# Kernel optimization log

Measured on AMD Instinct MI355X. Metric: run time of the kernel, lower is better.

## Reference

```python
import math
import jax, jax.numpy as jnp
import numpy as np

NUM_HEADS = 16
EMBED = 1024
B, T = 2, 2048


def setup_inputs() -> dict:
    key = jax.random.key(0)
    k1, k2 = jax.random.split(key)
    x = jax.random.normal(k1, (B, T, EMBED), dtype=jnp.float32)
    # kaiming-uniform-style init for [num_heads*embed, embed]
    bound = 1.0 / math.sqrt(NUM_HEADS * EMBED)
    weight = jax.random.uniform(k2, (NUM_HEADS * EMBED, EMBED), dtype=jnp.float32,
                                minval=-bound, maxval=bound)
    return {"x": x, "weight": weight}


def reference(x, weight):
    b, t, c = x.shape
    nh = NUM_HEADS
    hs = c // nh
    # b t (nh hs) -> b nh t hs
    y = x.reshape(b, t, nh, hs).transpose(0, 2, 1, 3)
    # scores: [b, nh, t, t], scaled by sqrt(hs) (yt.shape[-2] == hs)
    scores = jnp.einsum('bhtk,bhsk->bhts', y, y) / math.sqrt(hs)
    attn = jax.nn.softmax(scores, axis=-1)
    # value is raw x broadcast per head; contract without materializing the repeat
    o = jnp.einsum('bhts,bsc->bhtc', attn, x)          # [b, nh, t, c]
    o = o.transpose(0, 2, 1, 3).reshape(b, t, nh * c)  # b nh t c -> b t (nh c)
    return o @ weight                                   # [b, t, c]
```

## Files before the change

### kernel.cpp

```cpp
#include <hip/hip_runtime.h>
#include <hip/hip_bf16.h>


typedef __hip_bfloat16 bf16;
typedef __bf16 bf16x8 __attribute__((ext_vector_type(8)));
typedef float f32x4 __attribute__((ext_vector_type(4)));

#define B_ 2
#define T_ 2048
#define C_ 1024
#define H_ 16
#define D_ 16384
#define E_ 1024
#define KZ_ 8

__device__ __forceinline__ void load_lds16(const void* g, void* l) {
  __builtin_amdgcn_global_load_lds(
      (const __attribute__((address_space(1))) void*)g,
      (__attribute__((address_space(3))) void*)l, 16, 0, 0);
}

__device__ __forceinline__ unsigned pack2(float a, float b) {
  union { bf16 h[2]; unsigned u; } p;
  p.h[0] = __float2bfloat16(a);
  p.h[1] = __float2bfloat16(b);
  return p.u;
}

__global__ __launch_bounds__(256) void transpose_cast_kernel(
    const float* __restrict__ in, bf16* __restrict__ out, int rows, int cols) {
  __shared__ float tile[32][33];
  size_t zoff = (size_t)blockIdx.z * rows * cols;
  int c0 = blockIdx.x * 32, r0 = blockIdx.y * 32;
  int tx = threadIdx.x, ty = threadIdx.y;
  for (int i = ty; i < 32; i += 8)
    tile[i][tx] = in[zoff + (size_t)(r0 + i) * cols + c0 + tx];
  __syncthreads();
  for (int i = ty; i < 32; i += 8)
    out[zoff + (size_t)(c0 + i) * rows + r0 + tx] = __float2bfloat16(tile[tx][i]);
}

__global__ __launch_bounds__(256) void xh_cast_kernel(
    const float* __restrict__ x, bf16* __restrict__ xh) {
  int bt = blockIdx.x;
  int b = bt >> 11, t = bt & (T_ - 1);
  float4 v = ((const float4*)(x + (size_t)bt * C_))[threadIdx.x];
  int c = threadIdx.x * 4;
  int h = c >> 6, k = c & 63;
  bf16* o = xh + ((size_t)(b * H_ + h) * T_ + t) * 64 + k;
  o[0] = __float2bfloat16(v.x);
  o[1] = __float2bfloat16(v.y);
  o[2] = __float2bfloat16(v.z);
  o[3] = __float2bfloat16(v.w);
}

__global__ __launch_bounds__(256) void reduce_kernel(
    const bf16* __restrict__ p, float* __restrict__ out, int n8) {
  int i = blockIdx.x * 256 + threadIdx.x;
  if (i >= n8) return;
  float a[8] = {};
#pragma unroll
  for (int z = 0; z < KZ_; ++z) {
    bf16x8 v = ((const bf16x8*)(p + (size_t)z * n8 * 8))[i];
#pragma unroll
    for (int k = 0; k < 8; ++k) a[k] += (float)v[k];
  }
  float4 lo = make_float4(a[0], a[1], a[2], a[3]);
  float4 hi = make_float4(a[4], a[5], a[6], a[7]);
  ((float4*)out)[2 * i] = lo;
  ((float4*)out)[2 * i + 1] = hi;
}

__global__ __launch_bounds__(256) void scores_kernel(
    const bf16* __restrict__ xh,
    bf16* __restrict__ P,
    float* __restrict__ lsum) {
  int L = blockIdx.x;
  int z = blockIdx.y;
  int ti = 0, rem = L;
  while (rem >= H_ - ti) { rem -= H_ - ti; ++ti; }
  int tj = ti + rem;

  const bf16* A = xh + (size_t)z * T_ * 64;
  bf16* Pz = P + (size_t)z * T_ * T_;
  size_t row0 = (size_t)ti * 128, col0 = (size_t)tj * 128;

  __shared__ bf16 lds_a[128 * 64];
  __shared__ bf16 lds_b[128 * 64];
  int t = threadIdx.x;

  const bf16* ga = A + (row0 + (t >> 3)) * 64 + (t & 7) * 8;
  const bf16* gb = A + (col0 + (t >> 3)) * 64 + (t & 7) * 8;
#pragma unroll
  for (int q = 0; q < 4; ++q) {
    load_lds16(ga + q * 32 * 64, lds_a + t * 8 + q * 2048);
    load_lds16(gb + q * 32 * 64, lds_b + t * 8 + q * 2048);
  }
  __syncthreads();

  int lane = t & 63, w = t >> 6;
  int wm = (w & 1) * 64, wn = (w >> 1) * 64;
  int lr = lane & 15, lq = lane >> 4;
  const int a_off = (wm + lr) * 64 + lq * 8;
  const int b_off = (wn + lr) * 64 + lq * 8;

  f32x4 acc[4][4] = {};
#pragma unroll
  for (int kh = 0; kh < 2; ++kh) {
    bf16x8 af[4], bfr[4];
#pragma unroll
    for (int i = 0; i < 4; ++i)
      af[i] = *(const bf16x8*)&lds_a[a_off + kh * 32 + i * 16 * 64];
#pragma unroll
    for (int j = 0; j < 4; ++j)
      bfr[j] = *(const bf16x8*)&lds_b[b_off + kh * 32 + j * 16 * 64];
#pragma unroll
    for (int i = 0; i < 4; ++i)
#pragma unroll
      for (int j = 0; j < 4; ++j)
        acc[i][j] = __builtin_amdgcn_mfma_f32_16x16x32_bf16(af[i], bfr[j],
                                                            acc[i][j], 0, 0, 0);
  }

  float rs[4][4];
  float cs[4];
#pragma unroll
  for (int i2 = 0; i2 < 4; ++i2)
#pragma unroll
    for (int reg = 0; reg < 4; ++reg) rs[i2][reg] = 0.f;
#pragma unroll
  for (int j2 = 0; j2 < 4; ++j2) cs[j2] = 0.f;

#pragma unroll
  for (int i2 = 0; i2 < 4; ++i2) {
    size_t rb = row0 + wm + i2 * 16 + lq * 4;
#pragma unroll
    for (int j2 = 0; j2 < 4; ++j2) {
      size_t c = col0 + wn + j2 * 16 + lr;
      float e[4];
#pragma unroll
      for (int reg = 0; reg < 4; ++reg) {
        e[reg] = __expf(acc[i2][j2][reg] * 0.125f);
        rs[i2][reg] += e[reg];
        cs[j2] += e[reg];
        float nb = __shfl_xor(e[reg], 1);
        if ((lr & 1) == 0)
          *(unsigned*)&Pz[(rb + reg) * T_ + c] = pack2(e[reg], nb);
      }
      uint2 mv;
      mv.x = pack2(e[0], e[1]);
      mv.y = pack2(e[2], e[3]);
      *(uint2*)&Pz[c * T_ + rb] = mv;
    }
  }

#pragma unroll
  for (int i2 = 0; i2 < 4; ++i2)
#pragma unroll
    for (int reg = 0; reg < 4; ++reg) {
#pragma unroll
      for (int off = 1; off < 16; off <<= 1)
        rs[i2][reg] += __shfl_xor(rs[i2][reg], off);
    }
  if (lr == 0) {
#pragma unroll
    for (int i2 = 0; i2 < 4; ++i2) {
      size_t rb = row0 + wm + i2 * 16 + lq * 4;
#pragma unroll
      for (int reg = 0; reg < 4; ++reg)
        atomicAdd(&lsum[(size_t)z * T_ + rb + reg], rs[i2][reg]);
    }
  }
  if (ti != tj) {
#pragma unroll
    for (int j2 = 0; j2 < 4; ++j2) {
      cs[j2] += __shfl_xor(cs[j2], 16);
      cs[j2] += __shfl_xor(cs[j2], 32);
    }
    if (lq == 0) {
#pragma unroll
      for (int j2 = 0; j2 < 4; ++j2) {
        size_t c = col0 + wn + j2 * 16 + lr;
        atomicAdd(&lsum[(size_t)z * T_ + c], cs[j2]);
      }
    }
  }
}

template <int MODE, int SWZ>
__global__ __launch_bounds__(256, 4) void gemm_bt_kernel(
    const bf16* __restrict__ A, long long a_zstride, int lda,
    const bf16* __restrict__ BT, long long b_zstride, int ldb,
    void* __restrict__ Cout, int ldc, long long c_zflat,
    const float* __restrict__ lsum, int lzs, int K) {
  __shared__ bf16 lds_a[128 * 32];
  __shared__ bf16 lds_b[128 * 32];
  int t = threadIdx.x;

  int bx = blockIdx.x, by = blockIdx.y, bz = blockIdx.z;
  if (SWZ) {
    int gx = gridDim.x, gy = gridDim.y, gz = gridDim.z;
    int S = gy * gz, nb = gx * S;
    if (((S & 7) == 0) && ((nb & 7) == 0)) {
      int L = bx + gx * (by + gy * bz);
      int xcd = L & 7, m = L >> 3, spx = S >> 3;
      int col = m % gx, sl = m / gx;
      int strip = xcd * spx + sl;
      bx = col; by = strip % gy; bz = strip / gy;
    }
  }

  const bf16* Ab = A + (size_t)bz * a_zstride;
  const bf16* Bb = BT + (size_t)bz * b_zstride;
  size_t row0 = (size_t)by * 128;
  size_t col0 = (size_t)bx * 128;

  const bf16* ga = Ab + (row0 + (t >> 2)) * (size_t)lda + (t & 3) * 8;
  const bf16* gb = Bb + (col0 + (t >> 2)) * (size_t)ldb + (t & 3) * 8;
  bf16* la = lds_a + t * 8;
  bf16* lb = lds_b + t * 8;

  f32x4 acc[4][4] = {};
  int lane = t & 63;
  int w = t >> 6;
  int wm = (w & 1) * 64, wn = (w >> 1) * 64;
  int lr = lane & 15, lq = lane >> 4;
  const int a_off0 = (wm + lr) * 32 + lq * 8;
  const int b_off0 = (wn + lr) * 32 + lq * 8;

  for (int k0 = 0; k0 < K; k0 += 32) {
    load_lds16(ga, la);
    load_lds16(ga + 64 * (size_t)lda, la + 64 * 32);
    load_lds16(gb, lb);
    load_lds16(gb + 64 * (size_t)ldb, lb + 64 * 32);
    ga += 32;
    gb += 32;
    __syncthreads();

    bf16x8 af[4], bfr[4];
#pragma unroll
    for (int i = 0; i < 4; ++i)
      af[i] = *(const bf16x8*)&lds_a[a_off0 + i * 16 * 32];
#pragma unroll
    for (int j = 0; j < 4; ++j)
      bfr[j] = *(const bf16x8*)&lds_b[b_off0 + j * 16 * 32];
#pragma unroll
    for (int i = 0; i < 4; ++i)
#pragma unroll
      for (int j = 0; j < 4; ++j)
        acc[i][j] = __builtin_amdgcn_mfma_f32_16x16x32_bf16(af[i], bfr[j],
                                                            acc[i][j], 0, 0, 0);
    __syncthreads();
  }

  size_t cbase = (size_t)bz * c_zflat + col0;
#pragma unroll
  for (int i = 0; i < 4; ++i) {
    size_t r = row0 + wm + i * 16 + lq * 4;
    float4 inv4 = make_float4(1.f, 1.f, 1.f, 1.f);
    if (MODE == 3) {
      float4 lv = *(const float4*)&lsum[(size_t)bz * lzs + r];
      inv4 = make_float4(1.f / lv.x, 1.f / lv.y, 1.f / lv.z, 1.f / lv.w);
    }
#pragma unroll
    for (int j = 0; j < 4; ++j) {
      size_t c = cbase + wn + j * 16 + lr;
#pragma unroll
      for (int reg = 0; reg < 4; ++reg) {
        float v = acc[i][j][reg];
        if (MODE == 3) {
          float iv = reg == 0 ? inv4.x : reg == 1 ? inv4.y : reg == 2 ? inv4.z
                                                                      : inv4.w;
          v *= iv;
        }
        float nb = __shfl_xor(v, 1);
        if ((lr & 1) == 0) {
          size_t idx = (r + reg) * (size_t)ldc + c;
          *(unsigned*)&((bf16*)Cout)[idx] = pack2(v, nb);
        }
      }
    }
  }
}

extern "C" void kernel_launch(void* const* d_in, const int* in_sizes, int n_in,
                              void* d_out, int out_size, void* d_ws,
                              size_t ws_size, hipStream_t stream) {
  const float* x = (const float*)d_in[0];
  const float* wgt = (const float*)d_in[1];
  float* out = (float*)d_out;

  bf16* xbT = (bf16*)d_ws;
  bf16* wbT = xbT + (size_t)B_ * C_ * T_;
  bf16* xh = wbT + (size_t)E_ * D_;
  bf16* Obuf = xh + (size_t)B_ * H_ * T_ * 64;
  float* lsum = (float*)(Obuf + (size_t)B_ * T_ * D_);
  bf16* P = (bf16*)(lsum + (size_t)16 * T_);
  bf16* partials = P;

  transpose_cast_kernel<<<dim3(C_ / 32, T_ / 32, B_), dim3(32, 8), 0, stream>>>(
      x, xbT, T_, C_);
  transpose_cast_kernel<<<dim3(E_ / 32, D_ / 32, 1), dim3(32, 8), 0, stream>>>(
      wgt, wbT, D_, E_);
  xh_cast_kernel<<<B_ * T_, 256, 0, stream>>>(x, xh);

  size_t fixed_bytes = ((size_t)B_ * C_ * T_ + (size_t)E_ * D_ +
                        (size_t)B_ * H_ * T_ * 64 + (size_t)B_ * T_ * D_) * 2 +
                       (size_t)16 * T_ * 4;
  int Hs = 16;
  while (Hs > 1 && fixed_bytes + (size_t)Hs * T_ * T_ * 2 > ws_size) Hs >>= 1;

  for (int b = 0; b < B_; ++b) {
    for (int h0 = 0; h0 < H_; h0 += Hs) {
      const bf16* xhb = xh + (size_t)(b * H_ + h0) * T_ * 64;
      hipMemsetAsync(lsum, 0, (size_t)Hs * T_ * sizeof(float), stream);
      scores_kernel<<<dim3(136, Hs), 256, 0, stream>>>(xhb, P, lsum);
      gemm_bt_kernel<3, 1><<<dim3(C_ / 128, T_ / 128, Hs), 256, 0, stream>>>(
          P, (long long)T_ * T_, T_, xbT + (size_t)b * C_ * T_, 0LL, T_,
          (void*)(Obuf + (size_t)b * T_ * D_ + (size_t)h0 * C_), D_,
          (long long)C_, lsum, T_, T_);
    }
  }
  gemm_bt_kernel<1, 1><<<dim3(E_ / 128, (B_ * T_) / 128, KZ_), 256, 0,
                         stream>>>(Obuf, (long long)(D_ / KZ_), D_, wbT,
                                   (long long)(D_ / KZ_), D_, (void*)partials,
                                   E_, (long long)B_ * T_ * E_, nullptr, 0,
                                   D_ / KZ_);
  reduce_kernel<<<(B_ * T_ * E_ / 8 + 255) / 256, 256, 0, stream>>>(
      partials, out, B_ * T_ * E_ / 8);
}
```

Baseline: 759.0 us.

## Replace 128x128 GEMM with double-buffered 256x256 tile kernel using swizzled LDS

Result: no change. 744.2 us (-1.9%).

```diff
diff --git a/kernel.cpp b/kernel.cpp
--- a/kernel.cpp
+++ b/kernel.cpp
@@ -187,15 +187,76 @@
   }
 }
 
+template <int IH, int JH>
+__device__ __forceinline__ void quad(f32x4 (&acc)[8][4], const bf16x8 (&aR)[8],
+                                     const bf16x8 (&bR)[4]) {
+#pragma unroll
+  for (int i = 0; i < 4; ++i)
+#pragma unroll
+    for (int jj = 0; jj < 2; ++jj)
+#pragma unroll
+      for (int kk = 0; kk < 2; ++kk)
+        acc[IH * 4 + i][JH * 2 + jj] = __builtin_amdgcn_mfma_f32_16x16x32_bf16(
+            aR[i * 2 + kk], bR[jj * 2 + kk], acc[IH * 4 + i][JH * 2 + jj], 0, 0,
+            0);
+}
+
+#define STAGE_A(bufi, h, tau)                                                 \
+  do {                                                                        \
+    load_lds16(Ab + offA[(h)*2 + 0] + (tau)*64,                               \
+               &ldsA[bufi][(((h)*512) + t) * 8]);                             \
+    load_lds16(Ab + offA[(h)*2 + 1] + (tau)*64,                               \
+               &ldsA[bufi][((1024 + (h)*512) + t) * 8]);                      \
+  } while (0)
+
+#define STAGE_B(bufi, h, tau)                                                 \
+  do {                                                                        \
+    load_lds16(Bb + offB[(h)*2 + 0] + (tau)*64,                               \
+               &ldsB[bufi][(((t >> 8) * 512) + (h)*256 + (t & 255)) * 8]);    \
+    load_lds16(                                                               \
+        Bb + offB[(h)*2 + 1] + (tau)*64,                                      \
+        &ldsB[bufi][((((t + 512) >> 8) * 512) + (h)*256 + (t & 255)) * 8]);   \
+  } while (0)
+
+#define RD_A(dst, d, add)                                                     \
+  do {                                                                        \
+    dst[0] = *(const bf16x8*)&ldsA[d][aoff[0] + (add)];                       \
+    dst[1] = *(const bf16x8*)&ldsA[d][aoff[1] + (add)];                       \
+    dst[2] = *(const bf16x8*)&ldsA[d][aoff[2] + (add)];                       \
+    dst[3] = *(const bf16x8*)&ldsA[d][aoff[3] + (add)];                       \
+    dst[4] = *(const bf16x8*)&ldsA[d][aoff[4] + (add)];                       \
+    dst[5] = *(const bf16x8*)&ldsA[d][aoff[5] + (add)];                       \
+    dst[6] = *(const bf16x8*)&ldsA[d][aoff[6] + (add)];                       \
+    dst[7] = *(const bf16x8*)&ldsA[d][aoff[7] + (add)];                       \
+  } while (0)
+
+#define RD_B(dst, d, add)                                                     \
+  do {                                                                        \
+    dst[0] = *(const bf16x8*)&ldsB[d][boff[0] + (add)];                       \
+    dst[1] = *(const bf16x8*)&ldsB[d][boff[1] + (add)];                       \
+    dst[2] = *(const bf16x8*)&ldsB[d][boff[2] + (add)];                       \
+    dst[3] = *(const bf16x8*)&ldsB[d][boff[3] + (add)];                       \
+  } while (0)
+
+#define PHASE_SYNC()                                                          \
+  __builtin_amdgcn_sched_barrier(0);                                          \
+  __builtin_amdgcn_s_barrier();                                               \
+  asm volatile("s_waitcnt lgkmcnt(0)" ::: "memory");                          \
+  __builtin_amdgcn_sched_barrier(0)
+
+#define PHASE_END()                                                           \
+  __builtin_amdgcn_sched_barrier(0);                                          \
+  __builtin_amdgcn_s_barrier()
+
 template <int MODE, int SWZ>
-__global__ __launch_bounds__(256, 4) void gemm_bt_kernel(
+__global__ __launch_bounds__(512, 2) void gemm256_kernel(
     const bf16* __restrict__ A, long long a_zstride, int lda,
     const bf16* __restrict__ BT, long long b_zstride, int ldb,
     void* __restrict__ Cout, int ldc, long long c_zflat,
     const float* __restrict__ lsum, int lzs, int K) {
-  __shared__ bf16 lds_a[128 * 32];
-  __shared__ bf16 lds_b[128 * 32];
-  int t = threadIdx.x;
+  __shared__ __align__(16) bf16 ldsA[2][256 * 64];
+  __shared__ __align__(16) bf16 ldsB[2][256 * 64];
+  const int t = threadIdx.x;
 
   int bx = blockIdx.x, by = blockIdx.y, bz = blockIdx.z;
   if (SWZ) {
@@ -212,51 +273,100 @@
 
   const bf16* Ab = A + (size_t)bz * a_zstride;
   const bf16* Bb = BT + (size_t)bz * b_zstride;
-  size_t row0 = (size_t)by * 128;
-  size_t col0 = (size_t)bx * 128;
-
-  const bf16* ga = Ab + (row0 + (t >> 2)) * (size_t)lda + (t & 3) * 8;
-  const bf16* gb = Bb + (col0 + (t >> 2)) * (size_t)ldb + (t & 3) * 8;
-  bf16* la = lds_a + t * 8;
-  bf16* lb = lds_b + t * 8;
-
-  f32x4 acc[4][4] = {};
-  int lane = t & 63;
-  int w = t >> 6;
-  int wm = (w & 1) * 64, wn = (w >> 1) * 64;
-  int lr = lane & 15, lq = lane >> 4;
-  const int a_off0 = (wm + lr) * 32 + lq * 8;
-  const int b_off0 = (wn + lr) * 32 + lq * 8;
-
-  for (int k0 = 0; k0 < K; k0 += 32) {
-    load_lds16(ga, la);
-    load_lds16(ga + 64 * (size_t)lda, la + 64 * 32);
-    load_lds16(gb, lb);
-    load_lds16(gb + 64 * (size_t)ldb, lb + 64 * 32);
-    ga += 32;
-    gb += 32;
-    __syncthreads();
-
-    bf16x8 af[4], bfr[4];
-#pragma unroll
-    for (int i = 0; i < 4; ++i)
-      af[i] = *(const bf16x8*)&lds_a[a_off0 + i * 16 * 32];
-#pragma unroll
-    for (int j = 0; j < 4; ++j)
-      bfr[j] = *(const bf16x8*)&lds_b[b_off0 + j * 16 * 32];
-#pragma unroll
-    for (int i = 0; i < 4; ++i)
-#pragma unroll
-      for (int j = 0; j < 4; ++j)
-        acc[i][j] = __builtin_amdgcn_mfma_f32_16x16x32_bf16(af[i], bfr[j],
-                                                            acc[i][j], 0, 0, 0);
-    __syncthreads();
-  }
-
-  size_t cbase = (size_t)bz * c_zflat + col0;
-#pragma unroll
-  for (int i = 0; i < 4; ++i) {
-    size_t r = row0 + wm + i * 16 + lq * 4;
+  const size_t row0 = (size_t)by * 256;
+  const size_t col0 = (size_t)bx * 256;
+  const int NT = K >> 6;
+
+  int offA[4], offB[4];
+#pragma unroll
+  for (int h = 0; h < 2; ++h)
+#pragma unroll
+    for (int l = 0; l < 2; ++l) {
+      int s = h * 512 + l * 1024 + t;
+      int src = s ^ ((s >> 3) & 7);
+      offA[h * 2 + l] =
+          (int)((row0 + (size_t)(src >> 3)) * (size_t)lda) + (src & 7) * 8;
+      int u = t + l * 512;
+      int sb = (u >> 8) * 512 + h * 256 + (u & 255);
+      int srcb = sb ^ ((sb >> 3) & 7);
+      offB[h * 2 + l] =
+          (int)((col0 + (size_t)(srcb >> 3)) * (size_t)ldb) + (srcb & 7) * 8;
+    }
+
+  const int lane = t & 63, w = t >> 6;
+  const int wr = w >> 2, wc = w & 3;
+  const int lr = lane & 15, lq = lane >> 4;
+  const int axor = (lr & 7) << 3;
+  int aoff[8], boff[4];
+#pragma unroll
+  for (int i = 0; i < 4; ++i)
+#pragma unroll
+    for (int kk = 0; kk < 2; ++kk)
+      aoff[i * 2 + kk] =
+          (((wr * 128 + i * 16 + lr) * 64) + kk * 32 + lq * 8) ^ axor;
+#pragma unroll
+  for (int j = 0; j < 2; ++j)
+#pragma unroll
+    for (int kk = 0; kk < 2; ++kk)
+      boff[j * 2 + kk] =
+          (((wc * 64 + j * 16 + lr) * 64) + kk * 32 + lq * 8) ^ axor;
+
+  f32x4 acc[8][4] = {};
+  bf16x8 aR[8], bR0[4], bR1[4];
+
+  {
+    const int t1 = (NT > 1) ? 1 : 0;
+    STAGE_A(0, 0, 0);
+    STAGE_B(0, 0, 0);
+    STAGE_B(0, 1, 0);
+    STAGE_A(0, 1, 0);
+    STAGE_A(1, 0, t1);
+    STAGE_B(1, 0, t1);
+    STAGE_B(1, 1, t1);
+    asm volatile("s_waitcnt vmcnt(6)" ::: "memory");
+    __builtin_amdgcn_sched_barrier(0);
+    __builtin_amdgcn_s_barrier();
+  }
+
+  for (int tt = 0; tt < NT; ++tt) {
+    const int d = tt & 1, dn = d ^ 1;
+    const int tp1 = (tt + 1 < NT) ? (tt + 1) : (NT - 1);
+    const int tp2 = (tt + 2 < NT) ? (tt + 2) : (NT - 1);
+    RD_A(aR, d, 0);
+    RD_B(bR0, d, 0);
+    STAGE_A(dn, 1, tp1);
+    PHASE_SYNC();
+    __builtin_amdgcn_s_setprio(1);
+    quad<0, 0>(acc, aR, bR0);
+    __builtin_amdgcn_s_setprio(0);
+    PHASE_END();
+    RD_B(bR1, d, 2048);
+    STAGE_A(d, 0, tp2);
+    PHASE_SYNC();
+    __builtin_amdgcn_s_setprio(1);
+    quad<0, 1>(acc, aR, bR1);
+    __builtin_amdgcn_s_setprio(0);
+    PHASE_END();
+    RD_A(aR, d, 4096);
+    STAGE_B(d, 0, tp2);
+    PHASE_SYNC();
+    __builtin_amdgcn_s_setprio(1);
+    quad<1, 1>(acc, aR, bR1);
+    __builtin_amdgcn_s_setprio(0);
+    PHASE_END();
+    STAGE_B(d, 1, tp2);
+    asm volatile("s_waitcnt vmcnt(6)" ::: "memory");
+    PHASE_SYNC();
+    __builtin_amdgcn_s_setprio(1);
+    quad<1, 0>(acc, aR, bR0);
+    __builtin_amdgcn_s_setprio(0);
+    PHASE_END();
+  }
+
+  size_t cbase = (size_t)bz * c_zflat + col0 + wc * 64;
+#pragma unroll
+  for (int i = 0; i < 8; ++i) {
+    size_t r = row0 + wr * 128 + i * 16 + lq * 4;
     float4 inv4 = make_float4(1.f, 1.f, 1.f, 1.f);
     if (MODE == 3) {
       float4 lv = *(const float4*)&lsum[(size_t)bz * lzs + r];
@@ -264,7 +374,7 @@
     }
 #pragma unroll
     for (int j = 0; j < 4; ++j) {
-      size_t c = cbase + wn + j * 16 + lr;
+      size_t c = cbase + j * 16 + lr;
 #pragma unroll
       for (int reg = 0; reg < 4; ++reg) {
         float v = acc[i][j][reg];
@@ -315,13 +425,13 @@
       const bf16* xhb = xh + (size_t)(b * H_ + h0) * T_ * 64;
       hipMemsetAsync(lsum, 0, (size_t)Hs * T_ * sizeof(float), stream);
       scores_kernel<<<dim3(136, Hs), 256, 0, stream>>>(xhb, P, lsum);
-      gemm_bt_kernel<3, 1><<<dim3(C_ / 128, T_ / 128, Hs), 256, 0, stream>>>(
+      gemm256_kernel<3, 1><<<dim3(C_ / 256, T_ / 256, Hs), 512, 0, stream>>>(
           P, (long long)T_ * T_, T_, xbT + (size_t)b * C_ * T_, 0LL, T_,
           (void*)(Obuf + (size_t)b * T_ * D_ + (size_t)h0 * C_), D_,
           (long long)C_, lsum, T_, T_);
     }
   }
-  gemm_bt_kernel<1, 1><<<dim3(E_ / 128, (B_ * T_) / 128, KZ_), 256, 0,
+  gemm256_kernel<1, 1><<<dim3(E_ / 256, (B_ * T_) / 256, KZ_), 512, 0,
                          stream>>>(Obuf, (long long)(D_ / KZ_), D_, wbT,
                                    (long long)(D_ / KZ_), D_, (void*)partials,
                                    E_, (long long)B_ * T_ * E_, nullptr, 0,
```

## Double-buffer GEMM LDS tiles with K=64 steps and XOR-swizzled layout

Applied to the files above, without the earlier changes.

Result: slower. 793.4 us (+4.5%).

```diff
diff --git a/kernel.cpp b/kernel.cpp
--- a/kernel.cpp
+++ b/kernel.cpp
@@ -187,15 +187,47 @@
   }
 }
 
+#define STG_A(bufi, tau)                                                      \
+  do {                                                                        \
+    load_lds16(Ab + offA[0] + (size_t)(tau)*64, &ldsA[bufi][t * 8]);          \
+    load_lds16(Ab + offA[1] + (size_t)(tau)*64, &ldsA[bufi][(256 + t) * 8]);  \
+    load_lds16(Ab + offA[2] + (size_t)(tau)*64, &ldsA[bufi][(512 + t) * 8]);  \
+    load_lds16(Ab + offA[3] + (size_t)(tau)*64, &ldsA[bufi][(768 + t) * 8]);  \
+  } while (0)
+
+#define STG_B(bufi, tau)                                                      \
+  do {                                                                        \
+    load_lds16(Bb + offB[0] + (size_t)(tau)*64, &ldsB[bufi][t * 8]);          \
+    load_lds16(Bb + offB[1] + (size_t)(tau)*64, &ldsB[bufi][(256 + t) * 8]);  \
+    load_lds16(Bb + offB[2] + (size_t)(tau)*64, &ldsB[bufi][(512 + t) * 8]);  \
+    load_lds16(Bb + offB[3] + (size_t)(tau)*64, &ldsB[bufi][(768 + t) * 8]);  \
+  } while (0)
+
+#define RD4(dst, lds, off, kidx)                                              \
+  do {                                                                        \
+    dst[0] = *(const bf16x8*)&lds[off[0] + koff[kidx]];                       \
+    dst[1] = *(const bf16x8*)&lds[off[1] + koff[kidx]];                       \
+    dst[2] = *(const bf16x8*)&lds[off[2] + koff[kidx]];                       \
+    dst[3] = *(const bf16x8*)&lds[off[3] + koff[kidx]];                       \
+  } while (0)
+
+#define QUAD16()                                                              \
+  do {                                                                        \
+    _Pragma("unroll") for (int i = 0; i < 4; ++i)                             \
+        _Pragma("unroll") for (int j = 0; j < 4; ++j) acc[i][j] =             \
+        __builtin_amdgcn_mfma_f32_16x16x32_bf16(aR[i], bR[j], acc[i][j], 0,   \
+                                                0, 0);                        \
+  } while (0)
+
 template <int MODE, int SWZ>
-__global__ __launch_bounds__(256, 4) void gemm_bt_kernel(
+__global__ __launch_bounds__(256, 2) void gemm128_kernel(
     const bf16* __restrict__ A, long long a_zstride, int lda,
     const bf16* __restrict__ BT, long long b_zstride, int ldb,
     void* __restrict__ Cout, int ldc, long long c_zflat,
     const float* __restrict__ lsum, int lzs, int K) {
-  __shared__ bf16 lds_a[128 * 32];
-  __shared__ bf16 lds_b[128 * 32];
-  int t = threadIdx.x;
+  __shared__ __align__(16) bf16 ldsA[2][128 * 64];
+  __shared__ __align__(16) bf16 ldsB[2][128 * 64];
+  const int t = threadIdx.x;
 
   int bx = blockIdx.x, by = blockIdx.y, bz = blockIdx.z;
   if (SWZ) {
@@ -212,45 +244,53 @@
 
   const bf16* Ab = A + (size_t)bz * a_zstride;
   const bf16* Bb = BT + (size_t)bz * b_zstride;
-  size_t row0 = (size_t)by * 128;
-  size_t col0 = (size_t)bx * 128;
-
-  const bf16* ga = Ab + (row0 + (t >> 2)) * (size_t)lda + (t & 3) * 8;
-  const bf16* gb = Bb + (col0 + (t >> 2)) * (size_t)ldb + (t & 3) * 8;
-  bf16* la = lds_a + t * 8;
-  bf16* lb = lds_b + t * 8;
+  const size_t row0 = (size_t)by * 128;
+  const size_t col0 = (size_t)bx * 128;
+  const int NT = K >> 6;
+
+  int offA[4], offB[4];
+#pragma unroll
+  for (int l = 0; l < 4; ++l) {
+    int s = l * 256 + t;
+    int src = s ^ ((s >> 3) & 7);
+    offA[l] = (int)((row0 + (size_t)(src >> 3)) * (size_t)lda) + (src & 7) * 8;
+    offB[l] = (int)((col0 + (size_t)(src >> 3)) * (size_t)ldb) + (src & 7) * 8;
+  }
+
+  const int lane = t & 63, w = t >> 6;
+  const int wm = (w & 1) * 64, wn = (w >> 1) * 64;
+  const int lr = lane & 15, lq = lane >> 4;
+  const int axor = (lr & 7) << 3;
+  int aoff[4], boff[4], koff[2];
+  koff[0] = (lq * 8) ^ axor;
+  koff[1] = (32 + lq * 8) ^ axor;
+#pragma unroll
+  for (int i = 0; i < 4; ++i) {
+    aoff[i] = (wm + i * 16 + lr) * 64;
+    boff[i] = (wn + i * 16 + lr) * 64;
+  }
 
   f32x4 acc[4][4] = {};
-  int lane = t & 63;
-  int w = t >> 6;
-  int wm = (w & 1) * 64, wn = (w >> 1) * 64;
-  int lr = lane & 15, lq = lane >> 4;
-  const int a_off0 = (wm + lr) * 32 + lq * 8;
-  const int b_off0 = (wn + lr) * 32 + lq * 8;
-
-  for (int k0 = 0; k0 < K; k0 += 32) {
-    load_lds16(ga, la);
-    load_lds16(ga + 64 * (size_t)lda, la + 64 * 32);
-    load_lds16(gb, lb);
-    load_lds16(gb + 64 * (size_t)ldb, lb + 64 * 32);
-    ga += 32;
-    gb += 32;
-    __syncthreads();
-
-    bf16x8 af[4], bfr[4];
-#pragma unroll
-    for (int i = 0; i < 4; ++i)
-      af[i] = *(const bf16x8*)&lds_a[a_off0 + i * 16 * 32];
-#pragma unroll
-    for (int j = 0; j < 4; ++j)
-      bfr[j] = *(const bf16x8*)&lds_b[b_off0 + j * 16 * 32];
-#pragma unroll
-    for (int i = 0; i < 4; ++i)
-#pragma unroll
-      for (int j = 0; j < 4; ++j)
-        acc[i][j] = __builtin_amdgcn_mfma_f32_16x16x32_bf16(af[i], bfr[j],
-                                                            acc[i][j], 0, 0, 0);
-    __syncthreads();
+  bf16x8 aR[4], bR[4];
+
+  STG_A(0, 0);
+  STG_B(0, 0);
+  asm volatile("s_waitcnt vmcnt(0)" ::: "memory");
+  __builtin_amdgcn_s_barrier();
+
+  for (int tt = 0; tt < NT; ++tt) {
+    const int d = tt & 1, dn = d ^ 1;
+    const int tp1 = (tt + 1 < NT) ? (tt + 1) : tt;
+    RD4(aR, ldsA[d], aoff, 0);
+    RD4(bR, ldsB[d], boff, 0);
+    STG_A(dn, tp1);
+    QUAD16();
+    RD4(aR, ldsA[d], aoff, 1);
+    RD4(bR, ldsB[d], boff, 1);
+    STG_B(dn, tp1);
+    QUAD16();
+    asm volatile("s_waitcnt vmcnt(0)" ::: "memory");
+    __builtin_amdgcn_s_barrier();
   }
 
   size_t cbase = (size_t)bz * c_zflat + col0;
@@ -315,13 +355,13 @@
       const bf16* xhb = xh + (size_t)(b * H_ + h0) * T_ * 64;
       hipMemsetAsync(lsum, 0, (size_t)Hs * T_ * sizeof(float), stream);
       scores_kernel<<<dim3(136, Hs), 256, 0, stream>>>(xhb, P, lsum);
-      gemm_bt_kernel<3, 1><<<dim3(C_ / 128, T_ / 128, Hs), 256, 0, stream>>>(
+      gemm128_kernel<3, 1><<<dim3(C_ / 128, T_ / 128, Hs), 256, 0, stream>>>(
           P, (long long)T_ * T_, T_, xbT + (size_t)b * C_ * T_, 0LL, T_,
           (void*)(Obuf + (size_t)b * T_ * D_ + (size_t)h0 * C_), D_,
           (long long)C_, lsum, T_, T_);
     }
   }
-  gemm_bt_kernel<1, 1><<<dim3(E_ / 128, (B_ * T_) / 128, KZ_), 256, 0,
+  gemm128_kernel<1, 1><<<dim3(E_ / 128, (B_ * T_) / 128, KZ_), 256, 0,
                          stream>>>(Obuf, (long long)(D_ / KZ_), D_, wbT,
                                    (long long)(D_ / KZ_), D_, (void*)partials,
                                    E_, (long long)B_ * T_ * E_, nullptr, 0,
```
